# Kernel optimization log

Hardware: AMD Instinct MI355X
Metric: run time of the kernel (lower is better)

## Reference

```python
import jax, jax.numpy as jnp
import numpy as np

CAPACITY = 1024


def setup_inputs() -> dict:
    T, H, I, E, K = 2048, 1024, 1408, 8, 2
    key = jax.random.key(0)
    k0, k1, k2, k3, k4 = jax.random.split(key, 5)
    hidden_states = jax.random.normal(k0, (T, H), dtype=jnp.float32)
    w1 = jax.random.normal(k1, (E, 2 * I, H), dtype=jnp.float32) * 0.02  # [gate; up]
    w2 = jax.random.normal(k2, (E, H, I), dtype=jnp.float32) * 0.02
    topk_weights = jax.random.uniform(k3, (T, K), dtype=jnp.float32)
    topk_ids = jax.random.randint(k4, (T, K), 0, E, dtype=jnp.int32)
    return {"hidden_states": hidden_states, "w1": w1, "w2": w2,
            "topk_weights": topk_weights, "topk_ids": topk_ids}


def reference(hidden_states, w1, w2, topk_weights, topk_ids):
    # MoE: prepare(dispatch) -> grouped expert GEMM (silu-gated MLP) -> finalize(combine)
    T, H = hidden_states.shape
    E = w1.shape[0]
    I = w2.shape[2]
    K = topk_ids.shape[1]
    C = CAPACITY

    # ---- prepare: dispatch token copies to per-expert buffers ----
    flat_ids = topk_ids.reshape(-1)                       # (T*K,)
    onehot = jax.nn.one_hot(flat_ids, E, dtype=jnp.int32)  # (T*K, E)
    cs = jnp.cumsum(onehot, axis=0)                        # running per-expert counts
    pos = jnp.take_along_axis(cs, flat_ids[:, None], axis=1)[:, 0] - 1  # slot in expert buffer
    keep = pos < C
    pos_c = jnp.where(keep, pos, 0)

    x_flat = jnp.repeat(hidden_states, K, axis=0)          # (T*K, H)
    x_e = jnp.zeros((E, C, H), dtype=hidden_states.dtype)
    x_e = x_e.at[flat_ids, pos_c].add(jnp.where(keep[:, None], x_flat, 0.0))

    # ---- grouped expert GEMM: silu(gate) * up, then down-proj ----
    h = jnp.einsum('ech,eoh->eco', x_e, w1)                # (E, C, 2I)
    gate, up = h[..., :I], h[..., I:]
    act = jax.nn.silu(gate) * up                           # (E, C, I)
    y = jnp.einsum('eci,ehi->ech', act, w2)                # (E, C, H)

    # ---- finalize: gather back, apply router weights, reduce over top-k ----
    y_flat = y[flat_ids, pos_c] * (keep[:, None].astype(y.dtype)) \
             * topk_weights.reshape(-1, 1)                 # (T*K, H)
    out = y_flat.reshape(T, K, H).sum(axis=1)              # (T, H)
    return out.astype(hidden_states.dtype)
```

## Files before the change

kernel.cpp:

```cpp
#include <hip/hip_runtime.h>

#define NE 8
#define CAP 1024
#define HD 1024
#define ID 1408
#define TT 2048

typedef __attribute__((ext_vector_type(8))) short bf16x8;
typedef __attribute__((ext_vector_type(4))) float f32x4;
typedef unsigned short u16;
typedef unsigned int u32;
typedef unsigned long long u64;

__device__ __forceinline__ u16 f2bf(float f) {
  u32 u = __float_as_uint(f);
  u = (u + 0x7fffu + ((u >> 16) & 1u)) >> 16;
  return (u16)u;
}
__device__ __forceinline__ float bf2f(u16 b) {
  return __uint_as_float(((u32)b) << 16);
}

__device__ __forceinline__ void async_cp16(const void* g, void* l) {
  __builtin_amdgcn_global_load_lds(
      (const __attribute__((address_space(1))) u32*)g,
      (__attribute__((address_space(3))) u32*)l, 16, 0, 0);
}

__global__ void cvt_kernel(const float4* __restrict__ src, ushort4* __restrict__ dst, int n4) {
  int i = blockIdx.x * 256 + threadIdx.x;
  if (i >= n4) return;
  float4 v = src[i];
  ushort4 o;
  o.x = f2bf(v.x); o.y = f2bf(v.y); o.z = f2bf(v.z); o.w = f2bf(v.w);
  dst[i] = o;
}

__global__ void route_kernel(const int* __restrict__ ids, int* __restrict__ rowmap,
                             int* __restrict__ flatpos, int* __restrict__ counts) {
  __shared__ int ids_s[TT * 2];
  __shared__ int sc[256][NE + 1];
  int tid = threadIdx.x;
  for (int i = tid; i < TT * 2; i += 256) ids_s[i] = ids[i];
  __syncthreads();
  int base = tid * 16;
  u64 own64 = 0;
#pragma unroll
  for (int j = 0; j < 16; ++j) own64 += 1ull << (ids_s[base + j] * 8);
  int own[NE];
#pragma unroll
  for (int e = 0; e < NE; ++e) { own[e] = (int)((own64 >> (e * 8)) & 0xff); sc[tid][e] = own[e]; }
  __syncthreads();
  for (int off = 1; off < 256; off <<= 1) {
    int v[NE];
    if (tid >= off) {
#pragma unroll
      for (int e = 0; e < NE; ++e) v[e] = sc[tid - off][e];
    }
    __syncthreads();
    if (tid >= off) {
#pragma unroll
      for (int e = 0; e < NE; ++e) sc[tid][e] += v[e];
    }
    __syncthreads();
  }
  if (tid == 255) {
#pragma unroll
    for (int e = 0; e < NE; ++e) counts[e] = sc[255][e] < CAP ? sc[255][e] : CAP;
  }
  int excl[NE];
#pragma unroll
  for (int e = 0; e < NE; ++e) excl[e] = sc[tid][e] - own[e];
  __syncthreads();
#pragma unroll
  for (int e = 0; e < NE; ++e) sc[tid][e] = excl[e];
#pragma unroll
  for (int j = 0; j < 16; ++j) {
    int f = base + j;
    int e = ids_s[f];
    int p = sc[tid][e]++;
    if (p < CAP) { rowmap[e * CAP + p] = f; flatpos[f] = p; }
    else flatpos[f] = -1;
  }
}

template <bool GATHER>
__global__ __launch_bounds__(256) void gemm_bt(
    const u16* __restrict__ A, const u16* __restrict__ B, u16* __restrict__ C,
    const int* __restrict__ rowmap, const int* __restrict__ counts,
    int KE, int Astride, long long Bexp, int Cstride) {
  int e = blockIdx.x;
  int count = counts[e];
  int m0 = blockIdx.y * 128;
  if (m0 >= count) return;
  int n0 = blockIdx.z * 128;
  int tid = threadIdx.x;
  int lane = tid & 63, wid = tid >> 6;
  int wm = wid >> 1, wn = wid & 1;
  int q = lane >> 4, lm = lane & 15;

  __shared__ __align__(16) char smA[128 * 128];
  __shared__ __align__(16) char smB[128 * 128];

  int rloc = tid >> 3;
  int chs = ((tid & 7) ^ (rloc & 7)) * 8;
  const u16* aP[4];
  const u16* bP[4];
#pragma unroll
  for (int i = 0; i < 4; ++i) {
    int row = rloc + 32 * i;
    if (GATHER) {
      int gr = m0 + row;
      int f = (gr < count) ? rowmap[e * CAP + gr] : 0;
      aP[i] = A + (size_t)(f >> 1) * Astride + chs;
    } else {
      aP[i] = A + ((size_t)e * CAP + m0 + row) * Astride + chs;
    }
    bP[i] = B + (size_t)e * Bexp + (size_t)(n0 + row) * KE + chs;
  }

  f32x4 zero = {0.f, 0.f, 0.f, 0.f};
  f32x4 acc[4][4];
#pragma unroll
  for (int mi = 0; mi < 4; ++mi)
#pragma unroll
    for (int ni = 0; ni < 4; ++ni) acc[mi][ni] = zero;

  int nkt = KE >> 6;
  for (int kt = 0; kt < nkt; ++kt) {
    int ko = kt * 64;
#pragma unroll
    for (int i = 0; i < 4; ++i) {
      async_cp16(aP[i] + ko, smA + (i * 256 + tid) * 16);
      async_cp16(bP[i] + ko, smB + (i * 256 + tid) * 16);
    }
    asm volatile("s_waitcnt vmcnt(0)" ::: "memory");
    __syncthreads();
#pragma unroll
    for (int s = 0; s < 2; ++s) {
      bf16x8 af[4], bfr[4];
#pragma unroll
      for (int mi = 0; mi < 4; ++mi) {
        int row = wm * 64 + mi * 16 + lm;
        af[mi] = *(const bf16x8*)(smA + row * 128 + (((s * 4 + q) ^ (lm & 7)) * 16));
      }
#pragma unroll
      for (int ni = 0; ni < 4; ++ni) {
        int row = wn * 64 + ni * 16 + lm;
        bfr[ni] = *(const bf16x8*)(smB + row * 128 + (((s * 4 + q) ^ (lm & 7)) * 16));
      }
#pragma unroll
      for (int mi = 0; mi < 4; ++mi)
#pragma unroll
        for (int ni = 0; ni < 4; ++ni)
          acc[mi][ni] = __builtin_amdgcn_mfma_f32_16x16x32_bf16(af[mi], bfr[ni], acc[mi][ni], 0, 0, 0);
    }
    __syncthreads();
  }

#pragma unroll
  for (int mi = 0; mi < 4; ++mi) {
#pragma unroll
    for (int ni = 0; ni < 4; ++ni) {
      int col = n0 + wn * 64 + ni * 16 + lm;
#pragma unroll
      for (int r = 0; r < 4; ++r) {
        int row = m0 + wm * 64 + mi * 16 + q * 4 + r;
        C[((size_t)e * CAP + row) * Cstride + col] = f2bf(acc[mi][ni][r]);
      }
    }
  }
}

struct alignas(16) us8 { u16 v[8]; };
__global__ void act_kernel(u16* __restrict__ h, const int* __restrict__ counts) {
  int e = blockIdx.y;
  int c = blockIdx.x;
  if (c >= counts[e]) return;
  int tid = threadIdx.x;
  if (tid >= ID / 8) return;
  u16* rowp = h + ((size_t)e * CAP + c) * (2 * ID);
  us8 g = *(const us8*)(rowp + tid * 8);
  us8 u = *(const us8*)(rowp + ID + tid * 8);
  us8 o;
#pragma unroll
  for (int j = 0; j < 8; ++j) {
    float gf = bf2f(g.v[j]);
    float uf = bf2f(u.v[j]);
    float a = gf / (1.f + __expf(-gf)) * uf;
    o.v[j] = f2bf(a);
  }
  *(us8*)(rowp + tid * 8) = o;
}

__global__ void combine_kernel(const float* __restrict__ tw, const int* __restrict__ ids,
                               const int* __restrict__ flatpos, const u16* __restrict__ y,
                               float* __restrict__ out) {
  int t = blockIdx.x;
  int tid = threadIdx.x;
  int h0 = tid * 4;
  float a0 = 0.f, a1 = 0.f, a2 = 0.f, a3 = 0.f;
#pragma unroll
  for (int k = 0; k < 2; ++k) {
    int f = t * 2 + k;
    int p = flatpos[f];
    if (p >= 0) {
      int e = ids[f];
      float w = tw[f];
      const u16* yr = y + ((size_t)e * CAP + p) * HD + h0;
      ushort4 v = *(const ushort4*)yr;
      a0 += w * bf2f(v.x);
      a1 += w * bf2f(v.y);
      a2 += w * bf2f(v.z);
      a3 += w * bf2f(v.w);
    }
  }
  float4 o = {a0, a1, a2, a3};
  *(float4*)(out + (size_t)t * HD + h0) = o;
}

extern "C" void kernel_launch(void* const* d_in, const int* in_sizes, int n_in,
                              void* d_out, int out_size, void* d_ws, size_t ws_size,
                              hipStream_t stream) {
  const float* hidden = (const float*)d_in[0];
  const float* w1 = (const float*)d_in[1];
  const float* w2 = (const float*)d_in[2];
  const float* tw = (const float*)d_in[3];
  const int* ids = (const int*)d_in[4];
  float* out = (float*)d_out;

  char* p = (char*)d_ws;
  auto alloc = [&](size_t b) { char* r = p; p += (b + 255) & ~(size_t)255; return r; };
  u16* bw1 = (u16*)alloc((size_t)NE * 2 * ID * HD * 2);
  u16* bw2 = (u16*)alloc((size_t)NE * HD * ID * 2);
  u16* bx = (u16*)alloc((size_t)TT * HD * 2);
  u16* hbuf = (u16*)alloc((size_t)NE * CAP * 2 * ID * 2);
  u16* ybuf = (u16*)alloc((size_t)NE * CAP * HD * 2);
  int* rowmap = (int*)alloc((size_t)NE * CAP * 4);
  int* flatpos = (int*)alloc((size_t)TT * 2 * 4);
  int* counts = (int*)alloc((size_t)NE * 4);

  int n4w1 = NE * 2 * ID * HD / 4;
  cvt_kernel<<<(n4w1 + 255) / 256, 256, 0, stream>>>((const float4*)w1, (ushort4*)bw1, n4w1);
  int n4w2 = NE * HD * ID / 4;
  cvt_kernel<<<(n4w2 + 255) / 256, 256, 0, stream>>>((const float4*)w2, (ushort4*)bw2, n4w2);
  int n4x = TT * HD / 4;
  cvt_kernel<<<(n4x + 255) / 256, 256, 0, stream>>>((const float4*)hidden, (ushort4*)bx, n4x);

  route_kernel<<<1, 256, 0, stream>>>(ids, rowmap, flatpos, counts);

  gemm_bt<true><<<dim3(NE, CAP / 128, 2 * ID / 128), 256, 0, stream>>>(
      bx, bw1, hbuf, rowmap, counts, HD, HD, (long long)2 * ID * HD, 2 * ID);

  act_kernel<<<dim3(CAP, NE), 256, 0, stream>>>(hbuf, counts);

  gemm_bt<false><<<dim3(NE, CAP / 128, HD / 128), 256, 0, stream>>>(
      hbuf, bw2, ybuf, rowmap, counts, ID, 2 * ID, (long long)HD * ID, HD);

  combine_kernel<<<TT, 256, 0, stream>>>(tw, ids, flatpos, ybuf, out);
}
```

Measured before the change: 289.2 us.

## Fuse SiLU gating into gate/up GEMM epilogue and combine into down GEMM via atomics

Interleaves gate and up rows of w1 during the bf16 conversion so each adjacent column pair in the first GEMM's output tile is a gate/up pair. The epilogue applies silu(gate)*up through a lane shuffle and writes a half-width activation buffer, which removes the separate activation kernel and halves that intermediate. The down-projection GEMM uses 64-row tiles and scatters router-weighted results straight into the output with float atomicAdd after a zero pass, replacing the bf16 y buffer and the combine kernel. The cost is atomic traffic, a summation order that can vary between runs, and strided 2-byte epilogue stores.

```diff
diff --git a/kernel.cpp b/kernel.cpp
--- a/kernel.cpp
+++ b/kernel.cpp
@@ -34,6 +34,22 @@
   ushort4 o;
   o.x = f2bf(v.x); o.y = f2bf(v.y); o.z = f2bf(v.z); o.w = f2bf(v.w);
   dst[i] = o;
+}
+
+__global__ void cvt_w1_kernel(const float4* __restrict__ src, ushort4* __restrict__ dst) {
+  int n = blockIdx.x;
+  int e = blockIdx.y;
+  int tid = threadIdx.x;
+  int np = (n < ID) ? (2 * n) : (2 * (n - ID) + 1);
+  float4 v = src[((size_t)e * 2 * ID + n) * (HD / 4) + tid];
+  ushort4 o;
+  o.x = f2bf(v.x); o.y = f2bf(v.y); o.z = f2bf(v.z); o.w = f2bf(v.w);
+  dst[((size_t)e * 2 * ID + np) * (HD / 4) + tid] = o;
+}
+
+__global__ void zero_kernel(float4* __restrict__ out, int n4) {
+  int i = blockIdx.x * 256 + threadIdx.x;
+  if (i < n4) out[i] = float4{0.f, 0.f, 0.f, 0.f};
 }
 
 __global__ void route_kernel(const int* __restrict__ ids, int* __restrict__ rowmap,
@@ -84,11 +100,9 @@
   }
 }
 
-template <bool GATHER>
-__global__ __launch_bounds__(256) void gemm_bt(
-    const u16* __restrict__ A, const u16* __restrict__ B, u16* __restrict__ C,
-    const int* __restrict__ rowmap, const int* __restrict__ counts,
-    int KE, int Astride, long long Bexp, int Cstride) {
+__global__ __launch_bounds__(256) void gemm1_kernel(
+    const u16* __restrict__ A, const u16* __restrict__ B, u16* __restrict__ Hb,
+    const int* __restrict__ rowmap, const int* __restrict__ counts) {
   int e = blockIdx.x;
   int count = counts[e];
   int m0 = blockIdx.y * 128;
@@ -109,14 +123,10 @@
 #pragma unroll
   for (int i = 0; i < 4; ++i) {
     int row = rloc + 32 * i;
-    if (GATHER) {
-      int gr = m0 + row;
-      int f = (gr < count) ? rowmap[e * CAP + gr] : 0;
-      aP[i] = A + (size_t)(f >> 1) * Astride + chs;
-    } else {
-      aP[i] = A + ((size_t)e * CAP + m0 + row) * Astride + chs;
-    }
-    bP[i] = B + (size_t)e * Bexp + (size_t)(n0 + row) * KE + chs;
+    int gr = m0 + row;
+    int f = (gr < count) ? rowmap[e * CAP + gr] : 0;
+    aP[i] = A + (size_t)(f >> 1) * HD + chs;
+    bP[i] = B + ((size_t)e * 2 * ID + n0 + row) * HD + chs;
   }
 
   f32x4 zero = {0.f, 0.f, 0.f, 0.f};
@@ -126,8 +136,7 @@
 #pragma unroll
     for (int ni = 0; ni < 4; ++ni) acc[mi][ni] = zero;
 
-  int nkt = KE >> 6;
-  for (int kt = 0; kt < nkt; ++kt) {
+  for (int kt = 0; kt < HD / 64; ++kt) {
     int ko = kt * 64;
 #pragma unroll
     for (int i = 0; i < 4; ++i) {
@@ -158,65 +167,111 @@
     __syncthreads();
   }
 
+  bool isGate = (lm & 1) == 0;
 #pragma unroll
   for (int mi = 0; mi < 4; ++mi) {
 #pragma unroll
     for (int ni = 0; ni < 4; ++ni) {
-      int col = n0 + wn * 64 + ni * 16 + lm;
+      int cOut = (n0 >> 1) + wn * 32 + ni * 8 + (lm >> 1);
 #pragma unroll
       for (int r = 0; r < 4; ++r) {
-        int row = m0 + wm * 64 + mi * 16 + q * 4 + r;
-        C[((size_t)e * CAP + row) * Cstride + col] = f2bf(acc[mi][ni][r]);
-      }
-    }
-  }
-}
-
-struct alignas(16) us8 { u16 v[8]; };
-__global__ void act_kernel(u16* __restrict__ h, const int* __restrict__ counts) {
-  int e = blockIdx.y;
-  int c = blockIdx.x;
-  if (c >= counts[e]) return;
+        float v = acc[mi][ni][r];
+        float partner = __shfl_xor(v, 1, 64);
+        if (isGate) {
+          float g = v, u = partner;
+          float a = g / (1.f + __expf(-g)) * u;
+          int row = m0 + wm * 64 + mi * 16 + q * 4 + r;
+          Hb[((size_t)e * CAP + row) * ID + cOut] = f2bf(a);
+        }
+      }
+    }
+  }
+}
+
+__global__ __launch_bounds__(256) void gemm2_kernel(
+    const u16* __restrict__ A, const u16* __restrict__ B, float* __restrict__ out,
+    const int* __restrict__ rowmap, const int* __restrict__ counts,
+    const float* __restrict__ tw) {
+  int e = blockIdx.x;
+  int count = counts[e];
+  int m0 = blockIdx.y * 64;
+  if (m0 >= count) return;
+  int n0 = blockIdx.z * 128;
   int tid = threadIdx.x;
-  if (tid >= ID / 8) return;
-  u16* rowp = h + ((size_t)e * CAP + c) * (2 * ID);
-  us8 g = *(const us8*)(rowp + tid * 8);
-  us8 u = *(const us8*)(rowp + ID + tid * 8);
-  us8 o;
-#pragma unroll
-  for (int j = 0; j < 8; ++j) {
-    float gf = bf2f(g.v[j]);
-    float uf = bf2f(u.v[j]);
-    float a = gf / (1.f + __expf(-gf)) * uf;
-    o.v[j] = f2bf(a);
-  }
-  *(us8*)(rowp + tid * 8) = o;
-}
-
-__global__ void combine_kernel(const float* __restrict__ tw, const int* __restrict__ ids,
-                               const int* __restrict__ flatpos, const u16* __restrict__ y,
-                               float* __restrict__ out) {
-  int t = blockIdx.x;
-  int tid = threadIdx.x;
-  int h0 = tid * 4;
-  float a0 = 0.f, a1 = 0.f, a2 = 0.f, a3 = 0.f;
-#pragma unroll
-  for (int k = 0; k < 2; ++k) {
-    int f = t * 2 + k;
-    int p = flatpos[f];
-    if (p >= 0) {
-      int e = ids[f];
-      float w = tw[f];
-      const u16* yr = y + ((size_t)e * CAP + p) * HD + h0;
-      ushort4 v = *(const ushort4*)yr;
-      a0 += w * bf2f(v.x);
-      a1 += w * bf2f(v.y);
-      a2 += w * bf2f(v.z);
-      a3 += w * bf2f(v.w);
-    }
-  }
-  float4 o = {a0, a1, a2, a3};
-  *(float4*)(out + (size_t)t * HD + h0) = o;
+  int lane = tid & 63, wid = tid >> 6;
+  int wm = wid >> 1, wn = wid & 1;
+  int q = lane >> 4, lm = lane & 15;
+
+  __shared__ __align__(16) char smA[64 * 128];
+  __shared__ __align__(16) char smB[128 * 128];
+
+  int rloc = tid >> 3;
+  int chs = ((tid & 7) ^ (rloc & 7)) * 8;
+  const u16* aP[2];
+  const u16* bP[4];
+#pragma unroll
+  for (int i = 0; i < 2; ++i)
+    aP[i] = A + ((size_t)e * CAP + m0 + rloc + 32 * i) * ID + chs;
+#pragma unroll
+  for (int i = 0; i < 4; ++i)
+    bP[i] = B + ((size_t)e * HD + n0 + rloc + 32 * i) * ID + chs;
+
+  f32x4 zero = {0.f, 0.f, 0.f, 0.f};
+  f32x4 acc[2][4];
+#pragma unroll
+  for (int mi = 0; mi < 2; ++mi)
+#pragma unroll
+    for (int ni = 0; ni < 4; ++ni) acc[mi][ni] = zero;
+
+  for (int kt = 0; kt < ID / 64; ++kt) {
+    int ko = kt * 64;
+#pragma unroll
+    for (int i = 0; i < 2; ++i)
+      async_cp16(aP[i] + ko, smA + (i * 256 + tid) * 16);
+#pragma unroll
+    for (int i = 0; i < 4; ++i)
+      async_cp16(bP[i] + ko, smB + (i * 256 + tid) * 16);
+    asm volatile("s_waitcnt vmcnt(0)" ::: "memory");
+    __syncthreads();
+#pragma unroll
+    for (int s = 0; s < 2; ++s) {
+      bf16x8 af[2], bfr[4];
+#pragma unroll
+      for (int mi = 0; mi < 2; ++mi) {
+        int row = wm * 32 + mi * 16 + lm;
+        af[mi] = *(const bf16x8*)(smA + row * 128 + (((s * 4 + q) ^ (lm & 7)) * 16));
+      }
+#pragma unroll
+      for (int ni = 0; ni < 4; ++ni) {
+        int row = wn * 64 + ni * 16 + lm;
+        bfr[ni] = *(const bf16x8*)(smB + row * 128 + (((s * 4 + q) ^ (lm & 7)) * 16));
+      }
+#pragma unroll
+      for (int mi = 0; mi < 2; ++mi)
+#pragma unroll
+        for (int ni = 0; ni < 4; ++ni)
+          acc[mi][ni] = __builtin_amdgcn_mfma_f32_16x16x32_bf16(af[mi], bfr[ni], acc[mi][ni], 0, 0, 0);
+    }
+    __syncthreads();
+  }
+
+#pragma unroll
+  for (int mi = 0; mi < 2; ++mi) {
+#pragma unroll
+    for (int r = 0; r < 4; ++r) {
+      int grow = m0 + wm * 32 + mi * 16 + q * 4 + r;
+      if (grow < count) {
+        int f = rowmap[e * CAP + grow];
+        float w = tw[f];
+        int t = f >> 1;
+#pragma unroll
+        for (int ni = 0; ni < 4; ++ni) {
+          int col = n0 + wn * 64 + ni * 16 + lm;
+          atomicAdd(&out[(size_t)t * HD + col], w * acc[mi][ni][r]);
+        }
+      }
+    }
+  }
 }
 
 extern "C" void kernel_launch(void* const* d_in, const int* in_sizes, int n_in,
@@ -234,14 +289,12 @@
   u16* bw1 = (u16*)alloc((size_t)NE * 2 * ID * HD * 2);
   u16* bw2 = (u16*)alloc((size_t)NE * HD * ID * 2);
   u16* bx = (u16*)alloc((size_t)TT * HD * 2);
-  u16* hbuf = (u16*)alloc((size_t)NE * CAP * 2 * ID * 2);
-  u16* ybuf = (u16*)alloc((size_t)NE * CAP * HD * 2);
+  u16* hbuf = (u16*)alloc((size_t)NE * CAP * ID * 2);
   int* rowmap = (int*)alloc((size_t)NE * CAP * 4);
   int* flatpos = (int*)alloc((size_t)TT * 2 * 4);
   int* counts = (int*)alloc((size_t)NE * 4);
 
-  int n4w1 = NE * 2 * ID * HD / 4;
-  cvt_kernel<<<(n4w1 + 255) / 256, 256, 0, stream>>>((const float4*)w1, (ushort4*)bw1, n4w1);
+  cvt_w1_kernel<<<dim3(2 * ID, NE), 256, 0, stream>>>((const float4*)w1, (ushort4*)bw1);
   int n4w2 = NE * HD * ID / 4;
   cvt_kernel<<<(n4w2 + 255) / 256, 256, 0, stream>>>((const float4*)w2, (ushort4*)bw2, n4w2);
   int n4x = TT * HD / 4;
@@ -249,13 +302,12 @@
 
   route_kernel<<<1, 256, 0, stream>>>(ids, rowmap, flatpos, counts);
 
-  gemm_bt<true><<<dim3(NE, CAP / 128, 2 * ID / 128), 256, 0, stream>>>(
-      bx, bw1, hbuf, rowmap, counts, HD, HD, (long long)2 * ID * HD, 2 * ID);
-
-  act_kernel<<<dim3(CAP, NE), 256, 0, stream>>>(hbuf, counts);
-
-  gemm_bt<false><<<dim3(NE, CAP / 128, HD / 128), 256, 0, stream>>>(
-      hbuf, bw2, ybuf, rowmap, counts, ID, 2 * ID, (long long)HD * ID, HD);
-
-  combine_kernel<<<TT, 256, 0, stream>>>(tw, ids, flatpos, ybuf, out);
-}
+  int n4o = TT * HD / 4;
+  zero_kernel<<<(n4o + 255) / 256, 256, 0, stream>>>((float4*)out, n4o);
+
+  gemm1_kernel<<<dim3(NE, CAP / 128, 2 * ID / 128), 256, 0, stream>>>(
+      bx, bw1, hbuf, rowmap, counts);
+
+  gemm2_kernel<<<dim3(NE, CAP / 64, HD / 128), 256, 0, stream>>>(
+      hbuf, bw2, out, rowmap, counts, tw);
+}
```

Measured after the change: 292.3 us. About the same (+1.1%).
